# Kernel tuning notes

Measured on AMD Instinct MI355X. Metric: run time of the kernel, lower is better.

The kernel has to match this reference:

```python
import jax, jax.numpy as jnp
import numpy as np

B, L, G, D = 32, 128, 64, 256
HD = 128; H = 2 * HD          # bidirectional LSTM hidden
N, K = 8, 4                   # nodes per graph, idx per node
NINP, NHID, NREL = 128, 32, 16
NTOK = 1000
E = B * N * N                 # all-pairs edges per graph, flattened
EPS = 1e-5


def setup_inputs() -> dict:
    key = jax.random.key(0)
    ks = jax.random.split(key, 40)
    rn = lambda i, shape, s: (s * jax.random.normal(ks[i], shape)).astype(jnp.float32)
    inp = {}
    inp["seq"] = jax.random.randint(ks[0], (B, L), 0, NTOK, dtype=jnp.int32)
    inp["pos2grp"] = jax.random.randint(ks[1], (B, L), 0, G, dtype=jnp.int32)
    inp["idx"] = jax.random.randint(ks[2], (B, N, K), 0, L, dtype=jnp.int32)
    ii = np.repeat(np.arange(N), N); jj = np.tile(np.arange(N), N)
    inp["u"] = jnp.asarray((np.arange(B)[:, None] * N + ii[None, :]).reshape(-1), dtype=jnp.int32)
    inp["v"] = jnp.asarray((np.arange(B)[:, None] * N + jj[None, :]).reshape(-1), dtype=jnp.int32)
    inp["mask"] = jax.random.uniform(ks[3], (E, NREL)) < 0.1
    inp["emb"] = rn(4, (NTOK, D), 1.0)
    # BiLSTM params (1 layer, 2 directions); gate order i,f,g,o
    inp["Wih_f"] = rn(5, (4 * HD, D), 0.05); inp["Whh_f"] = rn(6, (4 * HD, HD), 0.05)
    inp["bih_f"] = jnp.zeros((4 * HD,), jnp.float32); inp["bhh_f"] = jnp.zeros((4 * HD,), jnp.float32)
    inp["Wih_b"] = rn(7, (4 * HD, D), 0.05); inp["Whh_b"] = rn(8, (4 * HD, HD), 0.05)
    inp["bih_b"] = jnp.zeros((4 * HD,), jnp.float32); inp["bhh_b"] = jnp.zeros((4 * HD,), jnp.float32)
    inp["lin_src_w"] = rn(9, (NINP, H), 0.05); inp["lin_src_b"] = jnp.zeros((NINP,), jnp.float32)
    inp["lin_dst_w"] = rn(10, (NINP, H), 0.05); inp["lin_dst_b"] = jnp.zeros((NINP,), jnp.float32)
    inp["bn_src_g"] = jnp.ones((NINP,), jnp.float32); inp["bn_src_b"] = jnp.zeros((NINP,), jnp.float32)
    inp["bn_dst_g"] = jnp.ones((NINP,), jnp.float32); inp["bn_dst_b"] = jnp.zeros((NINP,), jnp.float32)
    inp["ntl_w"] = rn(11, (NREL, NHID, NINP, NINP), 0.001)
    inp["ntl_v"] = rn(12, (NREL, NHID, 2 * NINP), 0.001)
    inp["ntl_b"] = jnp.zeros((NREL, NHID, 1), jnp.float32)
    inp["ntl_u"] = rn(13, (NREL, 1, NHID), 0.001)
    inp["ntl_bn_g"] = jnp.ones((NREL * NHID,), jnp.float32)
    inp["ntl_bn_b"] = jnp.zeros((NREL * NHID,), jnp.float32)
    return inp


def _lstm(xs, Wih, Whh, bih, bhh):
    # xs: (T, B, D) -> (T, B, HD)
    nb = xs.shape[1]
    def step(carry, xt):
        h, c = carry
        g = xt @ Wih.T + h @ Whh.T + bih + bhh
        i, f, gg, o = jnp.split(g, 4, axis=-1)
        c = jax.nn.sigmoid(f) * c + jax.nn.sigmoid(i) * jnp.tanh(gg)
        h = jax.nn.sigmoid(o) * jnp.tanh(c)
        return (h, c), h
    init = (jnp.zeros((nb, HD), xs.dtype), jnp.zeros((nb, HD), xs.dtype))
    _, hs = jax.lax.scan(step, init, xs)
    return hs


def _bn(x, g, b):
    # training-mode BatchNorm1d over axis 0 (biased variance, as torch)
    m = x.mean(0)
    v = x.var(0)
    return (x - m) * jax.lax.rsqrt(v + EPS) * g + b


def _forward(emb, Wih_f, Whh_f, bih_f, bhh_f, Wih_b, Whh_b, bih_b, bhh_b,
             lin_src_w, lin_src_b, lin_dst_w, lin_dst_b,
             bn_src_g, bn_src_b, bn_dst_g, bn_dst_b,
             ntl_w, ntl_v, ntl_b, ntl_u, ntl_bn_g, ntl_bn_b,
             seq, pos2grp, idx, u, v):
    # 1) token embedding + scatter_sum into groups
    x_tok = emb[seq]                                         # (B,L,D)
    flat_ids = (pos2grp + jnp.arange(B, dtype=pos2grp.dtype)[:, None] * G).reshape(-1)
    x_grp = jax.ops.segment_sum(x_tok.reshape(B * L, D), flat_ids,
                                num_segments=B * G).reshape(B, G, D)
    # 2) BiLSTM over group sequence
    xs = x_grp.transpose(1, 0, 2)                            # (G,B,D)
    hf = _lstm(xs, Wih_f, Whh_f, bih_f, bhh_f)
    hb = _lstm(xs[::-1], Wih_b, Whh_b, bih_b, bhh_b)[::-1]
    h_grp = jnp.concatenate([hf, hb], -1).transpose(1, 0, 2) # (B,G,H)
    # 3) fancy-indexed gather h_grp[i, pos2grp[i, idx], :] + scatter_sum over K
    grp_of_idx = jnp.take_along_axis(pos2grp, idx.reshape(B, N * K), axis=1)
    h_sel = jnp.take_along_axis(h_grp, grp_of_idx[..., None], axis=1)  # (B,N*K,H)
    h = h_sel.reshape(B, N, K, H).sum(2).reshape(B * N, H)
    # 4) per-endpoint projection + batchnorm
    hd = _bn(h[u] @ lin_src_w.T + lin_src_b, bn_src_g, bn_src_b)  # (E,NINP)
    tl = _bn(h[v] @ lin_dst_w.T + lin_dst_b, bn_dst_g, bn_dst_b)
    # 5) neural tensor layer (bilinear=True)
    cat = jnp.concatenate([hd, tl], 1)                       # (E,2*NINP)
    linear = jnp.einsum('rhi,ei->rhe', ntl_v, cat)
    tmp = jnp.einsum('rhij,ei->rhej', ntl_w, hd)             # (NREL,NHID,E,NINP)
    bilinear = jnp.einsum('rhej,ej->rhe', tmp, tl)
    pre = bilinear + linear + ntl_b                          # (NREL,NHID,E)
    flat = pre.reshape(NREL * NHID, E).T                     # (E, NREL*NHID)
    act = jnp.tanh(_bn(flat, ntl_bn_g, ntl_bn_b).T.reshape(NREL, NHID, E))
    logit = jnp.einsum('rh,rhe->er', ntl_u[:, 0, :], act)    # (E,NREL)
    return logit


def reference(seq, pos2grp, idx, u, v, mask, emb,
              Wih_f, Whh_f, bih_f, bhh_f, Wih_b, Whh_b, bih_b, bhh_b,
              lin_src_w, lin_src_b, lin_dst_w, lin_dst_b,
              bn_src_g, bn_src_b, bn_dst_g, bn_dst_b,
              ntl_w, ntl_v, ntl_b, ntl_u, ntl_bn_g, ntl_bn_b):
    logit = _forward(emb, Wih_f, Whh_f, bih_f, bhh_f, Wih_b, Whh_b, bih_b, bhh_b,
                     lin_src_w, lin_src_b, lin_dst_w, lin_dst_b,
                     bn_src_g, bn_src_b, bn_dst_g, bn_dst_b,
                     ntl_w, ntl_v, ntl_b, ntl_u, ntl_bn_g, ntl_bn_b,
                     seq, pos2grp, idx, u, v)
    gt = logit > 0
    eq = gt == mask
    acc = eq.astype(jnp.float32).mean()
    gid = jnp.repeat(jnp.arange(B, dtype=jnp.int32), N * N)
    em = jax.ops.segment_min(jnp.all(eq, 1).astype(jnp.int32), gid, num_segments=B)
    emr = em.astype(jnp.float32).mean()
    nll_pos = -jnp.sum(jnp.where(mask, jax.nn.log_sigmoid(logit), 0.0)) / B
    nll_neg = -jnp.sum(jnp.where(mask, 0.0, jnp.log(1.0 + 1e-5 - jax.nn.sigmoid(logit)))) / B
    loss = nll_pos + nll_neg
    return logit, loss, acc, emr
```

## Files before the change

kernel.cpp:

```cpp
#include <hip/hip_runtime.h>
#include <math.h>

namespace {

constexpr int cB = 32, cL = 128, cG = 64, cD = 256;
constexpr int cHD = 128, cH = 256;
constexpr int cN = 8, cK = 4;
constexpr int cNI = 128, cRH = 512;
constexpr int cE = 2048;
constexpr float cEPS = 1e-5f;

typedef __bf16 bf16x8 __attribute__((ext_vector_type(8)));
typedef float f32x4 __attribute__((ext_vector_type(4)));

__device__ __forceinline__ f32x4 mfma16(bf16x8 a, bf16x8 b, f32x4 c) {
    return __builtin_amdgcn_mfma_f32_16x16x32_bf16(a, b, c, 0, 0, 0);
}

__device__ __forceinline__ float bf2f(unsigned short u) {
    unsigned int x = ((unsigned int)u) << 16;
    return __uint_as_float(x);
}
__device__ __forceinline__ unsigned short f2bf(float f) {
    unsigned int x = __float_as_uint(f);
    unsigned int r = (x + 0x7fffu + ((x >> 16) & 1u)) >> 16;
    return (unsigned short)r;
}
__device__ __forceinline__ float frcp(float x) { return __builtin_amdgcn_rcpf(x); }
__device__ __forceinline__ float fsig(float x) { return frcp(1.f + __expf(-x)); }
__device__ __forceinline__ float ftanh(float x) { return 1.f - 2.f * frcp(__expf(2.f * x) + 1.f); }
__device__ __forceinline__ float nls(float x) {
    return (x >= 0.f) ? log1pf(expf(-x)) : (log1pf(expf(x)) - x);
}
__device__ __forceinline__ bf16x8 cvt8(const float* __restrict__ p) {
    float4 a = *(const float4*)p, b = *(const float4*)(p + 4);
    bf16x8 v;
    v[0] = (__bf16)a.x; v[1] = (__bf16)a.y; v[2] = (__bf16)a.z; v[3] = (__bf16)a.w;
    v[4] = (__bf16)b.x; v[5] = (__bf16)b.y; v[6] = (__bf16)b.z; v[7] = (__bf16)b.w;
    return v;
}

__device__ __forceinline__ void bar_lgkm() {
    asm volatile("s_waitcnt lgkmcnt(0)\n\ts_barrier" ::: "memory");
}

__global__ __launch_bounds__(256) void k_embed(
    const int* __restrict__ seq, const int* __restrict__ p2g,
    const float* __restrict__ emb, float* __restrict__ x_seq) {
    __shared__ float xl[cG * cD];
    __shared__ int toks[cL], grps[cL];
    int b = blockIdx.x, t = threadIdx.x;
    if (t < 128) toks[t] = seq[b * cL + t];
    else grps[t - 128] = p2g[b * cL + (t - 128)];
    for (int g = 0; g < cG; ++g) xl[g * cD + t] = 0.f;
    __syncthreads();
    for (int l = 0; l < cL; l += 4) {
        float v0 = emb[(size_t)toks[l + 0] * cD + t];
        float v1 = emb[(size_t)toks[l + 1] * cD + t];
        float v2 = emb[(size_t)toks[l + 2] * cD + t];
        float v3 = emb[(size_t)toks[l + 3] * cD + t];
        xl[grps[l + 0] * cD + t] += v0;
        xl[grps[l + 1] * cD + t] += v1;
        xl[grps[l + 2] * cD + t] += v2;
        xl[grps[l + 3] * cD + t] += v3;
    }
    for (int g = 0; g < cG; ++g)
        x_seq[(g * cB + b) * cD + t] = xl[g * cD + t];
}

__global__ __launch_bounds__(512) void k_gemm_in(
    const float* __restrict__ x_seq,
    const float* __restrict__ wih_f, const float* __restrict__ wih_b,
    const float* __restrict__ bih_f, const float* __restrict__ bhh_f,
    const float* __restrict__ bih_b, const float* __restrict__ bhh_b,
    float* __restrict__ pre) {
    int ns = blockIdx.x, g = blockIdx.y;
    int t = threadIdx.x;
    int w = t >> 6, l = t & 63, lc = l & 15, lk = l >> 4;
    int gn = ns * 128 + w * 16 + lc;
    const float* wrow = (gn < 512) ? (wih_f + (size_t)gn * cD)
                                   : (wih_b + (size_t)(gn - 512) * cD);
    const float* xb0 = x_seq + ((size_t)g * 32 + lc) * cD;
    const float* xb1 = x_seq + ((size_t)g * 32 + 16 + lc) * cD;
    f32x4 acc0 = {0.f, 0.f, 0.f, 0.f}, acc1 = {0.f, 0.f, 0.f, 0.f};
#pragma unroll
    for (int kf = 0; kf < 8; ++kf) {
        int ko = kf * 32 + lk * 8;
        bf16x8 a = cvt8(wrow + ko);
        bf16x8 b0 = cvt8(xb0 + ko);
        bf16x8 b1 = cvt8(xb1 + ko);
        acc0 = mfma16(a, b0, acc0);
        acc1 = mfma16(a, b1, acc1);
    }
    int nb = ns * 128 + w * 16 + lk * 4;
    float4 bv;
    if (nb < 512) {
        float4 u = *(const float4*)(bih_f + nb);
        float4 v = *(const float4*)(bhh_f + nb);
        bv = make_float4(u.x + v.x, u.y + v.y, u.z + v.z, u.w + v.w);
    } else {
        float4 u = *(const float4*)(bih_b + nb - 512);
        float4 v = *(const float4*)(bhh_b + nb - 512);
        bv = make_float4(u.x + v.x, u.y + v.y, u.z + v.z, u.w + v.w);
    }
    size_t base = ((size_t)g * 256 + (nb >> 2)) * 32;
    *(float4*)(pre + (base + lc) * 4) =
        make_float4(acc0[0] + bv.x, acc0[1] + bv.y, acc0[2] + bv.z, acc0[3] + bv.w);
    *(float4*)(pre + (base + 16 + lc) * 4) =
        make_float4(acc1[0] + bv.x, acc1[1] + bv.y, acc1[2] + bv.z, acc1[3] + bv.w);
}

__device__ __forceinline__ void lstm_step(
    f32x4 (&acc)[4], float (&cst)[4], const bf16x8 (&wf)[4][4],
    const unsigned short* __restrict__ hr, unsigned short* __restrict__ hw,
    const int (&rdo)[4], int wro,
    const float* __restrict__ preb, int gpre, bool dopre,
    unsigned short* __restrict__ hob, int g) {
    bf16x8 hf[4];
#pragma unroll
    for (int kf = 0; kf < 4; ++kf)
        hf[kf] = *(const bf16x8*)((const char*)hr + rdo[kf]);
#pragma unroll
    for (int kf = 0; kf < 4; ++kf)
#pragma unroll
        for (int q = 0; q < 4; ++q)
            acc[q] = mfma16(wf[q][kf], hf[kf], acc[q]);
    float hv[4];
#pragma unroll
    for (int r = 0; r < 4; ++r) {
        float ig = fsig(acc[0][r]);
        float fg = fsig(acc[1][r]);
        float gg = ftanh(acc[2][r]);
        float og = fsig(acc[3][r]);
        float cv = fg * cst[r] + ig * gg;
        cst[r] = cv;
        hv[r] = og * ftanh(cv);
    }
    if (dopre) {
#pragma unroll
        for (int q = 0; q < 4; ++q)
            acc[q] = *(const f32x4*)(preb + (size_t)gpre * 32768 + q * 4096);
    }
    unsigned int p0 = (unsigned int)f2bf(hv[0]) | ((unsigned int)f2bf(hv[1]) << 16);
    unsigned int p1 = (unsigned int)f2bf(hv[2]) | ((unsigned int)f2bf(hv[3]) << 16);
    *(uint2*)((char*)hw + wro) = make_uint2(p0, p1);
    *(uint2*)(hob + (size_t)g * 8192) = make_uint2(p0, p1);
    bar_lgkm();
}

__global__ __launch_bounds__(512, 2) void k_lstm_m(
    const float* __restrict__ pre,
    const float* __restrict__ whh_f, const float* __restrict__ whh_b,
    unsigned short* __restrict__ h_out) {
    __shared__ __align__(16) unsigned short hl[2][2048];
    int t = threadIdx.x;
    int w = t >> 6, l = t & 63, lc = l & 15, lk = l >> 4;
    int dir = blockIdx.x >> 1, bg = (blockIdx.x & 1) * 16;
    const float* whh = dir ? whh_b : whh_f;
    bf16x8 wf[4][4];
#pragma unroll
    for (int q = 0; q < 4; ++q) {
        int n = q * 128 + w * 16 + lc;
#pragma unroll
        for (int kf = 0; kf < 4; ++kf)
            wf[q][kf] = cvt8(whh + (size_t)n * 128 + kf * 32 + lk * 8);
    }
    *(uint2*)&hl[1][t * 4] = make_uint2(0u, 0u);
    const float* preb = pre + ((size_t)(dir * 128 + w * 4 + lk) * 32 + (bg + lc)) * 4;
    unsigned short* hob = h_out + ((size_t)(dir * 32 + bg + lc) * 128 + w * 16 + lk * 4);
    int rdo[4];
#pragma unroll
    for (int kf = 0; kf < 4; ++kf)
        rdo[kf] = (lc * 256 + kf * 64 + lk * 16) ^ (lc << 4);
    int wro = (lc * 256 + w * 32 + lk * 8) ^ (lc << 4);
    f32x4 accA[4], accB[4];
    float cst[4] = {0.f, 0.f, 0.f, 0.f};
    int g0 = dir ? 63 : 0;
    int sgn = dir ? -1 : 1;
#pragma unroll
    for (int q = 0; q < 4; ++q) accA[q] = *(const f32x4*)(preb + (size_t)g0 * 32768 + q * 4096);
#pragma unroll
    for (int q = 0; q < 4; ++q) accB[q] = *(const f32x4*)(preb + (size_t)(g0 + sgn) * 32768 + q * 4096);
    bar_lgkm();
    for (int s = 0; s < 64; s += 2) {
        int ga = g0 + sgn * s;
        lstm_step(accA, cst, wf, hl[1], hl[0], rdo, wro, preb, ga + 2 * sgn, s < 62, hob, ga);
        lstm_step(accB, cst, wf, hl[0], hl[1], rdo, wro, preb, ga + 3 * sgn, s < 61, hob, ga + sgn);
    }
}

__global__ __launch_bounds__(256) void k_gather(
    const int* __restrict__ idx, const int* __restrict__ p2g,
    const unsigned short* __restrict__ h_out, float* __restrict__ hsumT) {
    int bn = blockIdx.x;
    int b = bn >> 3;
    int t = threadIdx.x;
    int dirq = t >> 7, hh = t & 127;
    int l0 = idx[bn * cK + 0], l1 = idx[bn * cK + 1];
    int l2 = idx[bn * cK + 2], l3 = idx[bn * cK + 3];
    int g0 = p2g[b * cL + l0], g1 = p2g[b * cL + l1];
    int g2 = p2g[b * cL + l2], g3 = p2g[b * cL + l3];
    size_t ro = (size_t)(dirq * 32 + b) * 128 + hh;
    float a = bf2f(h_out[(size_t)g0 * 8192 + ro]) + bf2f(h_out[(size_t)g1 * 8192 + ro]) +
              bf2f(h_out[(size_t)g2 * 8192 + ro]) + bf2f(h_out[(size_t)g3 * 8192 + ro]);
    hsumT[(size_t)t * 256 + bn] = a;
}

__global__ __launch_bounds__(256) void k_proj_bn(
    const float* __restrict__ hsumT,
    const float* __restrict__ w_src, const float* __restrict__ b_src,
    const float* __restrict__ w_dst, const float* __restrict__ b_dst,
    const float* __restrict__ g_src, const float* __restrict__ bb_src,
    const float* __restrict__ g_dst, const float* __restrict__ bb_dst,
    float* __restrict__ hd_bn, float* __restrict__ tl_bn) {
    int which = blockIdx.x, c = blockIdx.y, t = threadIdx.x;
    __shared__ float ws[256];
    __shared__ float ssum[256], ssq[256];
    ws[t] = (which ? w_dst : w_src)[(size_t)c * cH + t];
    __syncthreads();
    float acc = (which ? b_dst : b_src)[c];
#pragma unroll 8
    for (int k = 0; k < cH; ++k)
        acc += ws[k] * hsumT[(size_t)k * 256 + t];
    ssum[t] = acc;
    ssq[t] = acc * acc;
    __syncthreads();
    for (int o = 128; o > 0; o >>= 1) {
        if (t < o) { ssum[t] += ssum[t + o]; ssq[t] += ssq[t + o]; }
        __syncthreads();
    }
    float mean = ssum[0] * (1.f / 256.f);
    float var = ssq[0] * (1.f / 256.f) - mean * mean;
    float gam = which ? g_dst[c] : g_src[c];
    float bet = which ? bb_dst[c] : bb_src[c];
    float scale = gam * rsqrtf(var + cEPS);
    (which ? tl_bn : hd_bn)[(size_t)t * cNI + c] = (acc - mean) * scale + bet;
}

__global__ __launch_bounds__(256, 2) void k_ntl_A(
    const float* __restrict__ hd_bn, const float* __restrict__ tl_bn,
    const float* __restrict__ ntl_w, const float* __restrict__ ntl_v,
    unsigned short* __restrict__ tmp,
    float* __restrict__ lsrc, float* __restrict__ ldst) {
    __shared__ __align__(16) unsigned short wl[128 * 128];
    __shared__ float vsh[256];
    int rh = blockIdx.x, t = threadIdx.x;
    int w = t >> 6, l = t & 63, lc = l & 15, lk = l >> 4;
    vsh[t] = ntl_v[(size_t)rh * 256 + t];
    {
        const float* wbase = ntl_w + (size_t)rh * 16384;
        int k = t >> 1, c0 = (t & 1) * 64;
        int sw = ((k >> 3) & 3) << 4;
#pragma unroll
        for (int u = 0; u < 8; ++u) {
            bf16x8 v = cvt8(wbase + k * 128 + c0 + u * 8);
            *(bf16x8*)((char*)wl + ((k * 256 + (c0 + u * 8) * 2) ^ sw)) = v;
        }
    }
    __syncthreads();
    {
        const float* hr = hd_bn + (size_t)t * cNI;
        const float* tr = tl_bn + (size_t)t * cNI;
        float a1 = 0.f, a2 = 0.f;
#pragma unroll 8
        for (int i = 0; i < cNI; i += 4) {
            float4 h4 = *(const float4*)(hr + i);
            float4 t4 = *(const float4*)(tr + i);
            a1 += h4.x * vsh[i] + h4.y * vsh[i + 1] + h4.z * vsh[i + 2] + h4.w * vsh[i + 3];
            a2 += t4.x * vsh[128 + i] + t4.y * vsh[128 + i + 1] + t4.z * vsh[128 + i + 2] + t4.w * vsh[128 + i + 3];
        }
        lsrc[(size_t)rh * 256 + t] = a1;
        ldst[(size_t)rh * 256 + t] = a2;
    }
    f32x4 acc[4][8] = {};
#pragma unroll
    for (int kf = 0; kf < 4; ++kf) {
        bf16x8 af[4];
#pragma unroll
        for (int mt = 0; mt < 4; ++mt) {
            int m = w * 64 + mt * 16 + lc;
            af[mt] = cvt8(hd_bn + (size_t)m * 128 + kf * 32 + lk * 8);
        }
#pragma unroll
        for (int nt = 0; nt < 8; ++nt) {
            int kb = (kf * 32 + lk * 8) * 256;
            int jb = (nt * 16 + lc) * 2;
            bf16x8 bv = *(const bf16x8*)((char*)wl + ((kb + jb) ^ (lk << 4)));
#pragma unroll
            for (int mt = 0; mt < 4; ++mt) acc[mt][nt] = mfma16(af[mt], bv, acc[mt][nt]);
        }
    }
#pragma unroll
    for (int mt = 0; mt < 4; ++mt) {
#pragma unroll
        for (int nt = 0; nt < 8; ++nt) {
            unsigned int lo = (unsigned int)f2bf(acc[mt][nt][0]) | ((unsigned int)f2bf(acc[mt][nt][1]) << 16);
            unsigned int hi = (unsigned int)f2bf(acc[mt][nt][2]) | ((unsigned int)f2bf(acc[mt][nt][3]) << 16);
            size_t off = (size_t)rh * 32768 + (size_t)((((w * 4 + mt) * 8 + nt) * 64 + l) * 4);
            *(uint2*)(tmp + off) = make_uint2(lo, hi);
        }
    }
}

__global__ __launch_bounds__(64) void k_ntl_B(
    const unsigned short* __restrict__ tmp, const float* __restrict__ tl_bn,
    const float* __restrict__ lsrc, const float* __restrict__ ldst,
    const float* __restrict__ ntl_b, float* __restrict__ pre2,
    float2* __restrict__ part2) {
    int bgid = blockIdx.x;
    int rh = blockIdx.y;
    int t = threadIdx.x;
    int n0 = bgid * 32;
    __shared__ float tm[32][132];
    __shared__ float tl[32][132];
    {
        const uint4* src = (const uint4*)(tmp + (size_t)rh * 32768 +
                                          (size_t)(bgid >> 1) * 8192 + (size_t)(bgid & 1) * 4096);
#pragma unroll
        for (int rep = 0; rep < 8; ++rep) {
            int q = t + rep * 64;
            uint4 uv = src[q];
            unsigned int wds[4] = {uv.x, uv.y, uv.z, uv.w};
            int e0 = q * 8;
#pragma unroll
            for (int ui = 0; ui < 4; ++ui) {
                int e = e0 + ui * 2;
                int mt_l = e >> 11;
                int nt = (e >> 8) & 7;
                int ln = (e >> 2) & 63;
                int r = e & 3;
                int m = mt_l * 16 + (ln >> 4) * 4 + r;
                int j = nt * 16 + (ln & 15);
                tm[m][j] = bf2f((unsigned short)(wds[ui] & 0xffff));
                tm[m + 1][j] = bf2f((unsigned short)(wds[ui] >> 16));
            }
        }
#pragma unroll
        for (int rep = 0; rep < 4; ++rep) {
            int tt = t + rep * 64;
            int r = tt >> 3;
            int c0 = (tt & 7) * 16;
            const float4* fsrc = (const float4*)(tl_bn + (size_t)(n0 + r) * cNI + c0);
            float4 f0 = fsrc[0], f1 = fsrc[1], f2v = fsrc[2], f3 = fsrc[3];
            float* frow = &tl[r][c0];
            frow[0] = f0.x; frow[1] = f0.y; frow[2] = f0.z; frow[3] = f0.w;
            frow[4] = f1.x; frow[5] = f1.y; frow[6] = f1.z; frow[7] = f1.w;
            frow[8] = f2v.x; frow[9] = f2v.y; frow[10] = f2v.z; frow[11] = f2v.w;
            frow[12] = f3.x; frow[13] = f3.y; frow[14] = f3.z; frow[15] = f3.w;
        }
    }
    __syncthreads();
    int b_l = t >> 4, i2 = (t >> 2) & 3, j2 = t & 3;
    const float* ta0 = &tm[b_l * 8 + i2][0];
    const float* ta1 = &tm[b_l * 8 + i2 + 4][0];
    const float* tb0 = &tl[b_l * 8 + j2][0];
    const float* tb1 = &tl[b_l * 8 + j2 + 4][0];
    float s00 = 0.f, s01 = 0.f, s10 = 0.f, s11 = 0.f;
#pragma unroll 4
    for (int k = 0; k < 128; ++k) {
        float a0 = ta0[k], a1 = ta1[k], b0 = tb0[k], b1 = tb1[k];
        s00 += a0 * b0; s01 += a0 * b1; s10 += a1 * b0; s11 += a1 * b1;
    }
    int bglob = bgid * 4 + b_l;
    float nb = ntl_b[rh];
    const float* ls = lsrc + (size_t)rh * 256 + bglob * 8;
    const float* ld = ldst + (size_t)rh * 256 + bglob * 8;
    float* pr = pre2 + (size_t)rh * cE + bgid * 256 + b_l * 64;
    float vs[4];
    vs[0] = s00 + ls[i2] + ld[j2] + nb;
    vs[1] = s01 + ls[i2] + ld[j2 + 4] + nb;
    vs[2] = s10 + ls[i2 + 4] + ld[j2] + nb;
    vs[3] = s11 + ls[i2 + 4] + ld[j2 + 4] + nb;
    pr[i2 * 8 + j2] = vs[0];
    pr[i2 * 8 + j2 + 4] = vs[1];
    pr[(i2 + 4) * 8 + j2] = vs[2];
    pr[(i2 + 4) * 8 + j2 + 4] = vs[3];
    float sm = vs[0] + vs[1] + vs[2] + vs[3];
    float sq = vs[0] * vs[0] + vs[1] * vs[1] + vs[2] * vs[2] + vs[3] * vs[3];
#pragma unroll
    for (int o = 32; o > 0; o >>= 1) {
        sm += __shfl_down(sm, o);
        sq += __shfl_down(sq, o);
    }
    if (t == 0) part2[(size_t)rh * 8 + bgid] = make_float2(sm, sq);
}

__global__ __launch_bounds__(256) void k_final(
    const float* __restrict__ pre2, const float2* __restrict__ part2,
    const float* __restrict__ g2, const float* __restrict__ b2,
    const float* __restrict__ ntl_u, const int* __restrict__ mask,
    float* __restrict__ out, float* __restrict__ part) {
    int r = blockIdx.y, et = blockIdx.x;
    int t = threadIdx.x;
    __shared__ float sc[32], sh[32];
    {
        int rh_l = t >> 3, slot = t & 7;
        int rh = r * 32 + rh_l;
        float2 pp = part2[(size_t)rh * 8 + slot];
        float S = pp.x, Q = pp.y;
        S += __shfl_xor(S, 1); Q += __shfl_xor(Q, 1);
        S += __shfl_xor(S, 2); Q += __shfl_xor(Q, 2);
        S += __shfl_xor(S, 4); Q += __shfl_xor(Q, 4);
        if (slot == 0) {
            float mean = S * (1.f / 2048.f);
            float var = Q * (1.f / 2048.f) - mean * mean;
            float scv = g2[rh] * rsqrtf(var + cEPS);
            sc[rh_l] = scv;
            sh[rh_l] = b2[rh] - mean * scv;
        }
    }
    __syncthreads();
    int e = et * 256 + t;
    float a = 0.f;
#pragma unroll
    for (int h = 0; h < 32; ++h) {
        int rh = r * 32 + h;
        float p = pre2[(size_t)rh * cE + e];
        a += ntl_u[rh] * ftanh(fmaf(p, sc[h], sh[h]));
    }
    out[(size_t)e * 16 + r] = a;
    int m = mask[(size_t)e * 16 + r];
    bool mb = (m != 0);
    bool eq = ((a > 0.f) == mb);
    float nll = mb ? nls(a) : -logf(1.f / (1.f + expf(a)) + 1e-5f);
    float corr = eq ? 1.f : 0.f;
    unsigned long long bal = __ballot(eq);
    float em = (bal == ~0ull) ? 1.f : 0.f;
#pragma unroll
    for (int o = 32; o > 0; o >>= 1) {
        nll += __shfl_down(nll, o);
        corr += __shfl_down(corr, o);
    }
    if ((t & 63) == 0) {
        int bg = et * 4 + (t >> 6);
        float* p = part + ((size_t)bg * 16 + r) * 4;
        p[0] = nll; p[1] = corr; p[2] = em;
    }
}

__global__ void k_loss_fin(const float* __restrict__ part, float* __restrict__ out) {
    int t = threadIdx.x;
    float nll = 0.f, corr = 0.f, em = 0.f;
    if (t < 32) {
        em = 1.f;
        for (int r = 0; r < 16; ++r) {
            const float* p = part + ((size_t)t * 16 + r) * 4;
            nll += p[0]; corr += p[1]; em = fminf(em, p[2]);
        }
    }
#pragma unroll
    for (int o = 32; o > 0; o >>= 1) {
        nll += __shfl_down(nll, o);
        corr += __shfl_down(corr, o);
        em += __shfl_down(em, o);
    }
    if (t == 0) {
        out[32768] = nll / 32.f;
        out[32769] = corr / 32768.f;
        out[32770] = em / 32.f;
    }
}

}

extern "C" void kernel_launch(void* const* d_in, const int* in_sizes, int n_in,
                              void* d_out, int out_size, void* d_ws, size_t ws_size,
                              hipStream_t stream) {
    (void)in_sizes; (void)n_in; (void)out_size; (void)ws_size;
    const int* seq = (const int*)d_in[0];
    const int* p2g = (const int*)d_in[1];
    const int* idx = (const int*)d_in[2];
    const int* mask = (const int*)d_in[5];
    const float* emb = (const float*)d_in[6];
    const float* wih_f = (const float*)d_in[7];
    const float* whh_f = (const float*)d_in[8];
    const float* bih_f = (const float*)d_in[9];
    const float* bhh_f = (const float*)d_in[10];
    const float* wih_b = (const float*)d_in[11];
    const float* whh_b = (const float*)d_in[12];
    const float* bih_b = (const float*)d_in[13];
    const float* bhh_b = (const float*)d_in[14];
    const float* lsw = (const float*)d_in[15];
    const float* lsb = (const float*)d_in[16];
    const float* ldw = (const float*)d_in[17];
    const float* ldb = (const float*)d_in[18];
    const float* bn_sg = (const float*)d_in[19];
    const float* bn_sb = (const float*)d_in[20];
    const float* bn_dg = (const float*)d_in[21];
    const float* bn_db = (const float*)d_in[22];
    const float* ntlw = (const float*)d_in[23];
    const float* ntlv = (const float*)d_in[24];
    const float* ntlb = (const float*)d_in[25];
    const float* ntlu = (const float*)d_in[26];
    const float* bn2g = (const float*)d_in[27];
    const float* bn2b = (const float*)d_in[28];
    float* out = (float*)d_out;
    char* ws = (char*)d_ws;

    float* x_seq = (float*)(ws + 0);
    float* pre = (float*)(ws + 2097152);
    unsigned short* tmp = (unsigned short*)(ws + 0);
    size_t off = 33554432;
    unsigned short* h_out = (unsigned short*)(ws + off); off += 1048576;
    float* hsumT = (float*)(ws + off); off += 262144;
    float* hd_bn = (float*)(ws + off); off += 131072;
    float* tl_bn = (float*)(ws + off); off += 131072;
    float* lsrc = (float*)(ws + off); off += 524288;
    float* ldst = (float*)(ws + off); off += 524288;
    float* pre2 = (float*)(ws + off); off += 4194304;
    float2* part2 = (float2*)(ws + off); off += 32768;
    float* part = (float*)(ws + off); off += 8192;

    k_embed<<<32, 256, 0, stream>>>(seq, p2g, emb, x_seq);
    k_gemm_in<<<dim3(8, 64), 512, 0, stream>>>(x_seq, wih_f, wih_b, bih_f, bhh_f, bih_b, bhh_b, pre);
    k_lstm_m<<<4, 512, 0, stream>>>(pre, whh_f, whh_b, h_out);
    k_gather<<<256, 256, 0, stream>>>(idx, p2g, h_out, hsumT);
    k_proj_bn<<<dim3(2, 128), 256, 0, stream>>>(hsumT, lsw, lsb, ldw, ldb,
                                                bn_sg, bn_sb, bn_dg, bn_db, hd_bn, tl_bn);
    k_ntl_A<<<512, 256, 0, stream>>>(hd_bn, tl_bn, ntlw, ntlv, tmp, lsrc, ldst);
    k_ntl_B<<<dim3(8, 512), 64, 0, stream>>>(tmp, tl_bn, lsrc, ldst, ntlb, pre2, part2);
    k_final<<<dim3(8, 16), 256, 0, stream>>>(pre2, part2, bn2g, bn2b, ntlu, mask, out, part);
    k_loss_fin<<<1, 64, 0, stream>>>(part, out);
}
```

Baseline: 178.1 us.

## Interleave forward and backward LSTM directions within one block

The recurrent LSTM kernel now has each block process both directions for its 16-batch slice, interleaving the two independent recurrences inside every step. Two blocks are launched instead of four. The aim is to hide the MFMA, LDS and transcendental latency of one direction's serial chain behind the other's, since the per-step recurrence is latency-bound. The cost is doubled register use for weights and accumulators, which risks spills under the 512-thread launch bound, and half as many blocks in flight.

```diff
diff --git a/kernel.cpp b/kernel.cpp
--- a/kernel.cpp
+++ b/kernel.cpp
@@ -110,41 +110,59 @@
         make_float4(acc1[0] + bv.x, acc1[1] + bv.y, acc1[2] + bv.z, acc1[3] + bv.w);
 }
 
-__device__ __forceinline__ void lstm_step(
-    f32x4 (&acc)[4], float (&cst)[4], const bf16x8 (&wf)[4][4],
-    const unsigned short* __restrict__ hr, unsigned short* __restrict__ hw,
+__device__ __forceinline__ void step2(
+    f32x4 (&a0)[4], f32x4 (&a1)[4], float (&c0)[4], float (&c1)[4],
+    const bf16x8 (&wf0)[4][4], const bf16x8 (&wf1)[4][4],
+    const unsigned short* __restrict__ hr0, unsigned short* __restrict__ hw0,
+    const unsigned short* __restrict__ hr1, unsigned short* __restrict__ hw1,
     const int (&rdo)[4], int wro,
-    const float* __restrict__ preb, int gpre, bool dopre,
-    unsigned short* __restrict__ hob, int g) {
-    bf16x8 hf[4];
-#pragma unroll
-    for (int kf = 0; kf < 4; ++kf)
-        hf[kf] = *(const bf16x8*)((const char*)hr + rdo[kf]);
-#pragma unroll
-    for (int kf = 0; kf < 4; ++kf)
-#pragma unroll
-        for (int q = 0; q < 4; ++q)
-            acc[q] = mfma16(wf[q][kf], hf[kf], acc[q]);
-    float hv[4];
+    const float* __restrict__ preb0, const float* __restrict__ preb1,
+    int gp0, int gp1, bool dopre,
+    unsigned short* __restrict__ hob0, unsigned short* __restrict__ hob1,
+    int g0, int g1) {
+    bf16x8 hf0[4], hf1[4];
+#pragma unroll
+    for (int kf = 0; kf < 4; ++kf) {
+        hf0[kf] = *(const bf16x8*)((const char*)hr0 + rdo[kf]);
+        hf1[kf] = *(const bf16x8*)((const char*)hr1 + rdo[kf]);
+    }
+#pragma unroll
+    for (int kf = 0; kf < 4; ++kf) {
+#pragma unroll
+        for (int q = 0; q < 4; ++q) {
+            a0[q] = mfma16(wf0[q][kf], hf0[kf], a0[q]);
+            a1[q] = mfma16(wf1[q][kf], hf1[kf], a1[q]);
+        }
+    }
+    float hv0[4], hv1[4];
 #pragma unroll
     for (int r = 0; r < 4; ++r) {
-        float ig = fsig(acc[0][r]);
-        float fg = fsig(acc[1][r]);
-        float gg = ftanh(acc[2][r]);
-        float og = fsig(acc[3][r]);
-        float cv = fg * cst[r] + ig * gg;
-        cst[r] = cv;
-        hv[r] = og * ftanh(cv);
+        float ig0 = fsig(a0[0][r]), ig1 = fsig(a1[0][r]);
+        float fg0 = fsig(a0[1][r]), fg1 = fsig(a1[1][r]);
+        float gg0 = ftanh(a0[2][r]), gg1 = ftanh(a1[2][r]);
+        float og0 = fsig(a0[3][r]), og1 = fsig(a1[3][r]);
+        float cv0 = fg0 * c0[r] + ig0 * gg0;
+        float cv1 = fg1 * c1[r] + ig1 * gg1;
+        c0[r] = cv0;
+        c1[r] = cv1;
+        hv0[r] = og0 * ftanh(cv0);
+        hv1[r] = og1 * ftanh(cv1);
     }
     if (dopre) {
 #pragma unroll
-        for (int q = 0; q < 4; ++q)
-            acc[q] = *(const f32x4*)(preb + (size_t)gpre * 32768 + q * 4096);
-    }
-    unsigned int p0 = (unsigned int)f2bf(hv[0]) | ((unsigned int)f2bf(hv[1]) << 16);
-    unsigned int p1 = (unsigned int)f2bf(hv[2]) | ((unsigned int)f2bf(hv[3]) << 16);
-    *(uint2*)((char*)hw + wro) = make_uint2(p0, p1);
-    *(uint2*)(hob + (size_t)g * 8192) = make_uint2(p0, p1);
+        for (int q = 0; q < 4; ++q) {
+            a0[q] = *(const f32x4*)(preb0 + (size_t)gp0 * 32768 + q * 4096);
+            a1[q] = *(const f32x4*)(preb1 + (size_t)gp1 * 32768 + q * 4096);
+        }
+    }
+    unsigned int p00 = (unsigned int)f2bf(hv0[0]) | ((unsigned int)f2bf(hv0[1]) << 16);
+    unsigned int p01 = (unsigned int)f2bf(hv0[2]) | ((unsigned int)f2bf(hv0[3]) << 16);
+    unsigned int p10 = (unsigned int)f2bf(hv1[0]) | ((unsigned int)f2bf(hv1[1]) << 16);
+    unsigned int p11 = (unsigned int)f2bf(hv1[2]) | ((unsigned int)f2bf(hv1[3]) << 16);
+    *(uint2*)((char*)hw0 + wro) = make_uint2(p00, p01);
+    *(uint2*)((char*)hw1 + wro) = make_uint2(p10, p11);
+    *(uint2*)(hob0 + (size_t)g0 * 8192) = make_uint2(p00, p01);
+    *(uint2*)(hob1 + (size_t)g1 * 8192) = make_uint2(p10, p11);
     bar_lgkm();
 }
 
@@ -152,40 +170,49 @@
     const float* __restrict__ pre,
     const float* __restrict__ whh_f, const float* __restrict__ whh_b,
     unsigned short* __restrict__ h_out) {
-    __shared__ __align__(16) unsigned short hl[2][2048];
+    __shared__ __align__(16) unsigned short hl0[2][2048];
+    __shared__ __align__(16) unsigned short hl1[2][2048];
     int t = threadIdx.x;
     int w = t >> 6, l = t & 63, lc = l & 15, lk = l >> 4;
-    int dir = blockIdx.x >> 1, bg = (blockIdx.x & 1) * 16;
-    const float* whh = dir ? whh_b : whh_f;
-    bf16x8 wf[4][4];
+    int bg = blockIdx.x * 16;
+    bf16x8 wf0[4][4], wf1[4][4];
 #pragma unroll
     for (int q = 0; q < 4; ++q) {
         int n = q * 128 + w * 16 + lc;
 #pragma unroll
-        for (int kf = 0; kf < 4; ++kf)
-            wf[q][kf] = cvt8(whh + (size_t)n * 128 + kf * 32 + lk * 8);
-    }
-    *(uint2*)&hl[1][t * 4] = make_uint2(0u, 0u);
-    const float* preb = pre + ((size_t)(dir * 128 + w * 4 + lk) * 32 + (bg + lc)) * 4;
-    unsigned short* hob = h_out + ((size_t)(dir * 32 + bg + lc) * 128 + w * 16 + lk * 4);
+        for (int kf = 0; kf < 4; ++kf) {
+            wf0[q][kf] = cvt8(whh_f + (size_t)n * 128 + kf * 32 + lk * 8);
+            wf1[q][kf] = cvt8(whh_b + (size_t)n * 128 + kf * 32 + lk * 8);
+        }
+    }
+    *(uint2*)&hl0[1][t * 4] = make_uint2(0u, 0u);
+    *(uint2*)&hl1[1][t * 4] = make_uint2(0u, 0u);
+    const float* preb0 = pre + ((size_t)(w * 4 + lk) * 32 + (bg + lc)) * 4;
+    const float* preb1 = pre + ((size_t)(128 + w * 4 + lk) * 32 + (bg + lc)) * 4;
+    unsigned short* hob0 = h_out + ((size_t)(bg + lc) * 128 + w * 16 + lk * 4);
+    unsigned short* hob1 = h_out + ((size_t)(32 + bg + lc) * 128 + w * 16 + lk * 4);
     int rdo[4];
 #pragma unroll
     for (int kf = 0; kf < 4; ++kf)
         rdo[kf] = (lc * 256 + kf * 64 + lk * 16) ^ (lc << 4);
     int wro = (lc * 256 + w * 32 + lk * 8) ^ (lc << 4);
-    f32x4 accA[4], accB[4];
-    float cst[4] = {0.f, 0.f, 0.f, 0.f};
-    int g0 = dir ? 63 : 0;
-    int sgn = dir ? -1 : 1;
-#pragma unroll
-    for (int q = 0; q < 4; ++q) accA[q] = *(const f32x4*)(preb + (size_t)g0 * 32768 + q * 4096);
-#pragma unroll
-    for (int q = 0; q < 4; ++q) accB[q] = *(const f32x4*)(preb + (size_t)(g0 + sgn) * 32768 + q * 4096);
+    f32x4 aA0[4], aB0[4], aA1[4], aB1[4];
+    float c0[4] = {0.f, 0.f, 0.f, 0.f}, c1[4] = {0.f, 0.f, 0.f, 0.f};
+#pragma unroll
+    for (int q = 0; q < 4; ++q) {
+        aA0[q] = *(const f32x4*)(preb0 + (size_t)0 * 32768 + q * 4096);
+        aA1[q] = *(const f32x4*)(preb1 + (size_t)63 * 32768 + q * 4096);
+        aB0[q] = *(const f32x4*)(preb0 + (size_t)1 * 32768 + q * 4096);
+        aB1[q] = *(const f32x4*)(preb1 + (size_t)62 * 32768 + q * 4096);
+    }
     bar_lgkm();
     for (int s = 0; s < 64; s += 2) {
-        int ga = g0 + sgn * s;
-        lstm_step(accA, cst, wf, hl[1], hl[0], rdo, wro, preb, ga + 2 * sgn, s < 62, hob, ga);
-        lstm_step(accB, cst, wf, hl[0], hl[1], rdo, wro, preb, ga + 3 * sgn, s < 61, hob, ga + sgn);
+        step2(aA0, aA1, c0, c1, wf0, wf1,
+              hl0[1], hl0[0], hl1[1], hl1[0], rdo, wro,
+              preb0, preb1, s + 2, 61 - s, s < 62, hob0, hob1, s, 63 - s);
+        step2(aB0, aB1, c0, c1, wf0, wf1,
+              hl0[0], hl0[1], hl1[0], hl1[1], rdo, wro,
+              preb0, preb1, s + 3, 60 - s, s < 61, hob0, hob1, s + 1, 62 - s);
     }
 }
 
@@ -513,7 +540,7 @@
 
     k_embed<<<32, 256, 0, stream>>>(seq, p2g, emb, x_seq);
     k_gemm_in<<<dim3(8, 64), 512, 0, stream>>>(x_seq, wih_f, wih_b, bih_f, bhh_f, bih_b, bhh_b, pre);
-    k_lstm_m<<<4, 512, 0, stream>>>(pre, whh_f, whh_b, h_out);
+    k_lstm_m<<<2, 512, 0, stream>>>(pre, whh_f, whh_b, h_out);
     k_gather<<<256, 256, 0, stream>>>(idx, p2g, h_out, hsumT);
     k_proj_bn<<<dim3(2, 128), 256, 0, stream>>>(hsumT, lsw, lsb, ldw, ldb,
                                                 bn_sg, bn_sb, bn_dg, bn_db, hd_bn, tl_bn);
```

After: 274.4 us. +54.0%, slower.

## Fuse NTL bilinear stages into one kernel with MFMA second contraction

Applied to the files above, without the earlier changes.

Merges k_ntl_A and k_ntl_B into one kernel. The intermediate hd·W product stays in LDS as bf16 instead of going through a global tmp buffer, and the per-pair contraction with tl now runs on MFMA using a new bf16 copy of tl_bn written by k_proj_bn. This removes a kernel launch, the global round trip of the intermediate, and the scalar FP32 dot products. In exchange the LDS footprint grows to 64KB per block, which may lower occupancy, and only the block-diagonal entries of each 16x16 MFMA tile are kept, so some MFMA work is wasted.

```diff
diff --git a/kernel.cpp b/kernel.cpp
--- a/kernel.cpp
+++ b/kernel.cpp
@@ -212,7 +212,8 @@
     const float* __restrict__ w_dst, const float* __restrict__ b_dst,
     const float* __restrict__ g_src, const float* __restrict__ bb_src,
     const float* __restrict__ g_dst, const float* __restrict__ bb_dst,
-    float* __restrict__ hd_bn, float* __restrict__ tl_bn) {
+    float* __restrict__ hd_bn, float* __restrict__ tl_bn,
+    unsigned short* __restrict__ tl_bf) {
     int which = blockIdx.x, c = blockIdx.y, t = threadIdx.x;
     __shared__ float ws[256];
     __shared__ float ssum[256], ssq[256];
@@ -234,19 +235,25 @@
     float gam = which ? g_dst[c] : g_src[c];
     float bet = which ? bb_dst[c] : bb_src[c];
     float scale = gam * rsqrtf(var + cEPS);
-    (which ? tl_bn : hd_bn)[(size_t)t * cNI + c] = (acc - mean) * scale + bet;
-}
-
-__global__ __launch_bounds__(256, 2) void k_ntl_A(
+    float val = (acc - mean) * scale + bet;
+    (which ? tl_bn : hd_bn)[(size_t)t * cNI + c] = val;
+    if (which) tl_bf[(size_t)t * cNI + c] = f2bf(val);
+}
+
+__global__ __launch_bounds__(256, 2) void k_ntl(
     const float* __restrict__ hd_bn, const float* __restrict__ tl_bn,
+    const unsigned short* __restrict__ tl_bf,
     const float* __restrict__ ntl_w, const float* __restrict__ ntl_v,
-    unsigned short* __restrict__ tmp,
-    float* __restrict__ lsrc, float* __restrict__ ldst) {
-    __shared__ __align__(16) unsigned short wl[128 * 128];
+    const float* __restrict__ ntl_b,
+    float* __restrict__ pre2, float2* __restrict__ part2) {
+    __shared__ __align__(16) unsigned short Tl[256 * 128];
     __shared__ float vsh[256];
+    __shared__ float lsl[256], ldl[256];
+    __shared__ float rs[8];
     int rh = blockIdx.x, t = threadIdx.x;
     int w = t >> 6, l = t & 63, lc = l & 15, lk = l >> 4;
     vsh[t] = ntl_v[(size_t)rh * 256 + t];
+    unsigned short* wl = Tl;
     {
         const float* wbase = ntl_w + (size_t)rh * 16384;
         int k = t >> 1, c0 = (t & 1) * 64;
@@ -269,8 +276,8 @@
             a1 += h4.x * vsh[i] + h4.y * vsh[i + 1] + h4.z * vsh[i + 2] + h4.w * vsh[i + 3];
             a2 += t4.x * vsh[128 + i] + t4.y * vsh[128 + i + 1] + t4.z * vsh[128 + i + 2] + t4.w * vsh[128 + i + 3];
         }
-        lsrc[(size_t)rh * 256 + t] = a1;
-        ldst[(size_t)rh * 256 + t] = a2;
+        lsl[t] = a1;
+        ldl[t] = a2;
     }
     f32x4 acc[4][8] = {};
 #pragma unroll
@@ -290,99 +297,61 @@
             for (int mt = 0; mt < 4; ++mt) acc[mt][nt] = mfma16(af[mt], bv, acc[mt][nt]);
         }
     }
+    __syncthreads();
 #pragma unroll
     for (int mt = 0; mt < 4; ++mt) {
 #pragma unroll
         for (int nt = 0; nt < 8; ++nt) {
-            unsigned int lo = (unsigned int)f2bf(acc[mt][nt][0]) | ((unsigned int)f2bf(acc[mt][nt][1]) << 16);
-            unsigned int hi = (unsigned int)f2bf(acc[mt][nt][2]) | ((unsigned int)f2bf(acc[mt][nt][3]) << 16);
-            size_t off = (size_t)rh * 32768 + (size_t)((((w * 4 + mt) * 8 + nt) * 64 + l) * 4);
-            *(uint2*)(tmp + off) = make_uint2(lo, hi);
-        }
-    }
-}
-
-__global__ __launch_bounds__(64) void k_ntl_B(
-    const unsigned short* __restrict__ tmp, const float* __restrict__ tl_bn,
-    const float* __restrict__ lsrc, const float* __restrict__ ldst,
-    const float* __restrict__ ntl_b, float* __restrict__ pre2,
-    float2* __restrict__ part2) {
-    int bgid = blockIdx.x;
-    int rh = blockIdx.y;
-    int t = threadIdx.x;
-    int n0 = bgid * 32;
-    __shared__ float tm[32][132];
-    __shared__ float tl[32][132];
-    {
-        const uint4* src = (const uint4*)(tmp + (size_t)rh * 32768 +
-                                          (size_t)(bgid >> 1) * 8192 + (size_t)(bgid & 1) * 4096);
-#pragma unroll
-        for (int rep = 0; rep < 8; ++rep) {
-            int q = t + rep * 64;
-            uint4 uv = src[q];
-            unsigned int wds[4] = {uv.x, uv.y, uv.z, uv.w};
-            int e0 = q * 8;
-#pragma unroll
-            for (int ui = 0; ui < 4; ++ui) {
-                int e = e0 + ui * 2;
-                int mt_l = e >> 11;
-                int nt = (e >> 8) & 7;
-                int ln = (e >> 2) & 63;
-                int r = e & 3;
-                int m = mt_l * 16 + (ln >> 4) * 4 + r;
-                int j = nt * 16 + (ln & 15);
-                tm[m][j] = bf2f((unsigned short)(wds[ui] & 0xffff));
-                tm[m + 1][j] = bf2f((unsigned short)(wds[ui] >> 16));
+#pragma unroll
+            for (int r = 0; r < 4; ++r) {
+                int row = w * 64 + mt * 16 + lk * 4 + r;
+                int col = nt * 16 + lc;
+                int byte = (row * 256 + col * 2) ^ ((row & 7) << 4);
+                *(unsigned short*)((char*)Tl + byte) = f2bf(acc[mt][nt][r]);
             }
         }
-#pragma unroll
-        for (int rep = 0; rep < 4; ++rep) {
-            int tt = t + rep * 64;
-            int r = tt >> 3;
-            int c0 = (tt & 7) * 16;
-            const float4* fsrc = (const float4*)(tl_bn + (size_t)(n0 + r) * cNI + c0);
-            float4 f0 = fsrc[0], f1 = fsrc[1], f2v = fsrc[2], f3 = fsrc[3];
-            float* frow = &tl[r][c0];
-            frow[0] = f0.x; frow[1] = f0.y; frow[2] = f0.z; frow[3] = f0.w;
-            frow[4] = f1.x; frow[5] = f1.y; frow[6] = f1.z; frow[7] = f1.w;
-            frow[8] = f2v.x; frow[9] = f2v.y; frow[10] = f2v.z; frow[11] = f2v.w;
-            frow[12] = f3.x; frow[13] = f3.y; frow[14] = f3.z; frow[15] = f3.w;
-        }
-    }
-    __syncthreads();
-    int b_l = t >> 4, i2 = (t >> 2) & 3, j2 = t & 3;
-    const float* ta0 = &tm[b_l * 8 + i2][0];
-    const float* ta1 = &tm[b_l * 8 + i2 + 4][0];
-    const float* tb0 = &tl[b_l * 8 + j2][0];
-    const float* tb1 = &tl[b_l * 8 + j2 + 4][0];
-    float s00 = 0.f, s01 = 0.f, s10 = 0.f, s11 = 0.f;
-#pragma unroll 4
-    for (int k = 0; k < 128; ++k) {
-        float a0 = ta0[k], a1 = ta1[k], b0 = tb0[k], b1 = tb1[k];
-        s00 += a0 * b0; s01 += a0 * b1; s10 += a1 * b0; s11 += a1 * b1;
-    }
-    int bglob = bgid * 4 + b_l;
+    }
+    __syncthreads();
     float nb = ntl_b[rh];
-    const float* ls = lsrc + (size_t)rh * 256 + bglob * 8;
-    const float* ld = ldst + (size_t)rh * 256 + bglob * 8;
-    float* pr = pre2 + (size_t)rh * cE + bgid * 256 + b_l * 64;
-    float vs[4];
-    vs[0] = s00 + ls[i2] + ld[j2] + nb;
-    vs[1] = s01 + ls[i2] + ld[j2 + 4] + nb;
-    vs[2] = s10 + ls[i2 + 4] + ld[j2] + nb;
-    vs[3] = s11 + ls[i2 + 4] + ld[j2 + 4] + nb;
-    pr[i2 * 8 + j2] = vs[0];
-    pr[i2 * 8 + j2 + 4] = vs[1];
-    pr[(i2 + 4) * 8 + j2] = vs[2];
-    pr[(i2 + 4) * 8 + j2 + 4] = vs[3];
-    float sm = vs[0] + vs[1] + vs[2] + vs[3];
-    float sq = vs[0] * vs[0] + vs[1] * vs[1] + vs[2] * vs[2] + vs[3] * vs[3];
+    float sm = 0.f, sq = 0.f;
+#pragma unroll
+    for (int p = 0; p < 4; ++p) {
+        int ti = w * 4 + p;
+        int arow = ti * 16 + lc;
+        f32x4 d = {0.f, 0.f, 0.f, 0.f};
+#pragma unroll
+        for (int kf = 0; kf < 4; ++kf) {
+            const char* ta = (const char*)Tl +
+                ((arow * 256 + (kf * 32 + lk * 8) * 2) ^ ((arow & 7) << 4));
+            bf16x8 a = *(const bf16x8*)ta;
+            bf16x8 b = *(const bf16x8*)(tl_bf + (size_t)arow * 128 + kf * 32 + lk * 8);
+            d = mfma16(a, b, d);
+        }
+        int jg = lc >> 3;
+#pragma unroll
+        for (int r = 0; r < 4; ++r) {
+            int i = lk * 4 + r;
+            if ((i >> 3) == jg) {
+                int e = (ti * 2 + jg) * 64 + (i & 7) * 8 + (lc & 7);
+                float v = d[r] + lsl[ti * 16 + i] + ldl[arow] + nb;
+                pre2[(size_t)rh * cE + e] = v;
+                sm += v;
+                sq += v * v;
+            }
+        }
+    }
 #pragma unroll
     for (int o = 32; o > 0; o >>= 1) {
         sm += __shfl_down(sm, o);
         sq += __shfl_down(sq, o);
     }
-    if (t == 0) part2[(size_t)rh * 8 + bgid] = make_float2(sm, sq);
+    if (l == 0) { rs[w] = sm; rs[4 + w] = sq; }
+    __syncthreads();
+    if (t == 0) {
+        float S = rs[0] + rs[1] + rs[2] + rs[3];
+        float Q = rs[4] + rs[5] + rs[6] + rs[7];
+        part2[rh] = make_float2(S, Q);
+    }
 }
 
 __global__ __launch_bounds__(256) void k_final(
@@ -393,21 +362,14 @@
     int r = blockIdx.y, et = blockIdx.x;
     int t = threadIdx.x;
     __shared__ float sc[32], sh[32];
-    {
-        int rh_l = t >> 3, slot = t & 7;
-        int rh = r * 32 + rh_l;
-        float2 pp = part2[(size_t)rh * 8 + slot];
-        float S = pp.x, Q = pp.y;
-        S += __shfl_xor(S, 1); Q += __shfl_xor(Q, 1);
-        S += __shfl_xor(S, 2); Q += __shfl_xor(Q, 2);
-        S += __shfl_xor(S, 4); Q += __shfl_xor(Q, 4);
-        if (slot == 0) {
-            float mean = S * (1.f / 2048.f);
-            float var = Q * (1.f / 2048.f) - mean * mean;
-            float scv = g2[rh] * rsqrtf(var + cEPS);
-            sc[rh_l] = scv;
-            sh[rh_l] = b2[rh] - mean * scv;
-        }
+    if (t < 32) {
+        int rh = r * 32 + t;
+        float2 pp = part2[rh];
+        float mean = pp.x * (1.f / 2048.f);
+        float var = pp.y * (1.f / 2048.f) - mean * mean;
+        float scv = g2[rh] * rsqrtf(var + cEPS);
+        sc[t] = scv;
+        sh[t] = b2[rh] - mean * scv;
     }
     __syncthreads();
     int e = et * 256 + t;
@@ -499,16 +461,14 @@
 
     float* x_seq = (float*)(ws + 0);
     float* pre = (float*)(ws + 2097152);
-    unsigned short* tmp = (unsigned short*)(ws + 0);
     size_t off = 33554432;
     unsigned short* h_out = (unsigned short*)(ws + off); off += 1048576;
     float* hsumT = (float*)(ws + off); off += 262144;
     float* hd_bn = (float*)(ws + off); off += 131072;
     float* tl_bn = (float*)(ws + off); off += 131072;
-    float* lsrc = (float*)(ws + off); off += 524288;
-    float* ldst = (float*)(ws + off); off += 524288;
+    unsigned short* tl_bf = (unsigned short*)(ws + off); off += 65536;
     float* pre2 = (float*)(ws + off); off += 4194304;
-    float2* part2 = (float2*)(ws + off); off += 32768;
+    float2* part2 = (float2*)(ws + off); off += 4096;
     float* part = (float*)(ws + off); off += 8192;
 
     k_embed<<<32, 256, 0, stream>>>(seq, p2g, emb, x_seq);
@@ -516,9 +476,8 @@
     k_lstm_m<<<4, 512, 0, stream>>>(pre, whh_f, whh_b, h_out);
     k_gather<<<256, 256, 0, stream>>>(idx, p2g, h_out, hsumT);
     k_proj_bn<<<dim3(2, 128), 256, 0, stream>>>(hsumT, lsw, lsb, ldw, ldb,
-                                                bn_sg, bn_sb, bn_dg, bn_db, hd_bn, tl_bn);
-    k_ntl_A<<<512, 256, 0, stream>>>(hd_bn, tl_bn, ntlw, ntlv, tmp, lsrc, ldst);
-    k_ntl_B<<<dim3(8, 512), 64, 0, stream>>>(tmp, tl_bn, lsrc, ldst, ntlb, pre2, part2);
+                                                bn_sg, bn_sb, bn_dg, bn_db, hd_bn, tl_bn, tl_bf);
+    k_ntl<<<512, 256, 0, stream>>>(hd_bn, tl_bn, tl_bf, ntlw, ntlv, ntlb, pre2, part2);
     k_final<<<dim3(8, 16), 256, 0, stream>>>(pre2, part2, bn2g, bn2b, ntlu, mask, out, part);
     k_loss_fin<<<1, 64, 0, stream>>>(part, out);
 }
```

New measurement: 156.4 us. -12.2%, faster.
